# Performance work log

Hardware: AMD Instinct MI355X
Metric: run time of the kernel (lower is better)

## Reference

```python
import jax, jax.numpy as jnp
import numpy as np

B, S, D, H = 2, 2048, 768, 12
Dh = D // H  # attention_head_size = 64
NEG = -1e9


def setup_inputs() -> dict:
    key = jax.random.key(0)
    ks = jax.random.split(key, 10)
    scale = 1.0 / np.sqrt(D).astype(np.float32)
    inp = {
        "hidden_states": jax.random.normal(ks[0], (B, S, D), jnp.float32),
        "Wq": jax.random.normal(ks[1], (D, D), jnp.float32) * scale,
        "bq": jnp.zeros((D,), jnp.float32),
        "Wk": jax.random.normal(ks[2], (D, D), jnp.float32) * scale,
        "bk": jnp.zeros((D,), jnp.float32),
        "Wv": jax.random.normal(ks[3], (D, D), jnp.float32) * scale,
        "bv": jnp.zeros((D,), jnp.float32),
        "Wo": jax.random.normal(ks[4], (D, D), jnp.float32) * scale,
        "bo": jnp.zeros((D,), jnp.float32),
        "mask": jax.random.randint(ks[5], (B, S), 0, 2).astype(bool),
    }
    return inp


def _heads(x):
    # [B,S,D] -> [B,H,S,Dh]
    return x.reshape(B, S, H, Dh).transpose(0, 2, 1, 3)


def reference(hidden_states, Wq, bq, Wk, bk, Wv, bv, Wo, bo, mask):
    q = _heads(hidden_states @ Wq + bq)
    k = _heads(hidden_states @ Wk + bk)
    v = _heads(hidden_states @ Wv + bv)

    # [B,H,S,S] raw scores
    scores = jnp.einsum("bhqd,bhkd->bhqk", q, k) / np.sqrt(Dh).astype(np.float32)

    # pairwise fg mask: [B,1,S,S]; True where both query and key tokens are fg
    am = mask[:, None, :, None] & mask[:, None, None, :]

    # fg softmax: bg pairs masked to -1e9; bg softmax: fg pairs masked to -1e9
    fg_probs = jax.nn.softmax(jnp.where(am, scores, NEG), axis=-1)
    bg_probs = jnp.where(am, NEG, scores)
    bg_probs = jax.nn.softmax(bg_probs, axis=-1)

    # stitch: take fg probs at fg pairs, bg probs elsewhere (replaces boolean scatter)
    probs = jnp.where(am, fg_probs, bg_probs)

    ctx = jnp.einsum("bhqk,bhkd->bhqd", probs, v)
    ctx = ctx.transpose(0, 2, 1, 3).reshape(B, S, D)
    return ctx @ Wo + bo
```

## Files before the change

### kernel.cpp

```cpp
#include <hip/hip_runtime.h>

typedef float f32x4 __attribute__((ext_vector_type(4)));
typedef short bf16x8 __attribute__((ext_vector_type(8)));

#define MFMA16(a, b, c) __builtin_amdgcn_mfma_f32_16x16x32_bf16((a), (b), (c), 0, 0, 0)
#define WAITV4() asm volatile("s_waitcnt vmcnt(4)" ::: "memory")
#define WAITV8() asm volatile("s_waitcnt vmcnt(8)" ::: "memory")
#define WAITV0() asm volatile("s_waitcnt vmcnt(0)" ::: "memory")
#define WAITL0() asm volatile("s_waitcnt lgkmcnt(0)" ::: "memory")
#define BARRIER() __builtin_amdgcn_s_barrier()
#define SCHED0() __builtin_amdgcn_sched_barrier(0)

constexpr int S_ = 2048;
constexpr int D_ = 768;
constexpr int H_ = 12;
constexpr int DH = 64;
constexpr int B_ = 2;
constexpr int M_ = B_ * S_;
constexpr int BH = B_ * H_;

typedef unsigned short u16;
typedef unsigned int u32;

__device__ __forceinline__ u16 f2bf(float f) {
  u32 u = __builtin_bit_cast(u32, f);
  u += 0x7fffu + ((u >> 16) & 1u);
  return (u16)(u >> 16);
}
__device__ __forceinline__ u32 pack2(float a, float b) {
  return (u32)f2bf(a) | ((u32)f2bf(b) << 16);
}
__device__ __forceinline__ u32 pack2r(float lo, float hi) {
  u32 a = __builtin_bit_cast(u32, lo) + 0x8000u;
  u32 b = __builtin_bit_cast(u32, hi) + 0x8000u;
  return __builtin_amdgcn_perm(b, a, 0x07060302u);
}

__device__ __forceinline__ void gload16(const void* g, void* l) {
  __builtin_amdgcn_global_load_lds((const __attribute__((address_space(1))) u32*)g,
                                   (__attribute__((address_space(3))) u32*)l, 16, 0, 0);
}

__global__ __launch_bounds__(256) void conv_bf16(const float* __restrict__ in,
                                                 u16* __restrict__ out) {
  int i = blockIdx.x * 256 + threadIdx.x;
  float4 v = ((const float4*)in)[i];
  uint2 r;
  r.x = pack2(v.x, v.y);
  r.y = pack2(v.z, v.w);
  ((uint2*)out)[i] = r;
}

__global__ __launch_bounds__(256) void conv_wT4(const float* __restrict__ Wq,
                                                const float* __restrict__ Wk,
                                                const float* __restrict__ Wv,
                                                const float* __restrict__ Wo,
                                                u16* __restrict__ wqkv,
                                                u16* __restrict__ wo) {
  __shared__ float t[32][33];
  int z = blockIdx.z;
  const float* w = z == 0 ? Wq : z == 1 ? Wk : z == 2 ? Wv : Wo;
  u16* wt = z == 3 ? wo : wqkv + (size_t)z * D_ * D_;
  int k0 = blockIdx.x << 5, n0 = blockIdx.y << 5;
  int x = threadIdx.x & 31, y = threadIdx.x >> 5;
#pragma unroll
  for (int j = 0; j < 4; ++j) t[y + 8 * j][x] = w[(size_t)(k0 + y + 8 * j) * D_ + n0 + x];
  __syncthreads();
#pragma unroll
  for (int j = 0; j < 4; ++j) wt[(size_t)(n0 + y + 8 * j) * D_ + k0 + x] = f2bf(t[x][y + 8 * j]);
}

__global__ __launch_bounds__(256) void canon_mask(const void* __restrict__ mraw,
                                                  float* __restrict__ fm,
                                                  u32* __restrict__ mw) {
  __shared__ int isBool;
  int tid = threadIdx.x;
  if (tid == 0) isBool = 0;
  __syncthreads();
  const int* mi = (const int*)mraw;
  int v = mi[tid];
  if (v != 0 && v != 1) atomicOr(&isBool, 1);
  __syncthreads();
  const unsigned char* mb = (const unsigned char*)mraw;
  int p = blockIdx.x * 256 + tid;
  int m0, m1;
  if (isBool) { m0 = mb[2 * p]; m1 = mb[2 * p + 1]; }
  else        { m0 = mi[2 * p]; m1 = mi[2 * p + 1]; }
  fm[2 * p] = (float)m0;
  fm[2 * p + 1] = (float)m1;
  mw[p] = (m0 ? 0xFFFFu : 0u) | (m1 ? 0xFFFF0000u : 0u);
}

template <int MODE>
__global__ __launch_bounds__(256, 2) void gemm128(const u16* __restrict__ A,
                                                  const u16* __restrict__ Wt,
                                                  const float* __restrict__ bq,
                                                  const float* __restrict__ bk,
                                                  const float* __restrict__ bv,
                                                  u16* __restrict__ oq,
                                                  u16* __restrict__ ok,
                                                  u16* __restrict__ ov,
                                                  float* __restrict__ of,
                                                  float qscale) {
  constexpr int NT = D_ / 64;
  __shared__ __align__(16) u16 lA[2][128 * 64];
  __shared__ __align__(16) u16 lB[2][128 * 64];
  const int tid = threadIdx.x, w = tid >> 6, lane = tid & 63;
  const int g = lane >> 4, c = lane & 15;
  const int m0 = blockIdx.x * 128, n0 = blockIdx.y * 128;
  const int wr = w >> 1, wc = w & 1;
  const int srow = lane >> 3, scb = ((lane & 7) * 16) ^ (srow << 4);
  const int sw = (c & 7) << 4;
  const char* Ab = (const char*)A + (size_t)m0 * (D_ * 2);
  const char* Bb = (const char*)Wt + (size_t)n0 * (D_ * 2);

  auto stage = [&](int buf, int t) {
    int k0b = t * 128;
#pragma unroll
    for (int a = 0; a < 4; ++a) {
      int rr = w * 32 + a * 8;
      gload16(Ab + (size_t)(rr + srow) * (D_ * 2) + k0b + scb, &lA[buf][rr * 64]);
      gload16(Bb + (size_t)(rr + srow) * (D_ * 2) + k0b + scb, &lB[buf][rr * 64]);
    }
  };

  f32x4 acc[4][4] = {};
  auto compute = [&](int buf) {
    const char* pa = (const char*)&lA[buf][0];
    const char* pb = (const char*)&lB[buf][0];
#pragma unroll
    for (int kk = 0; kk < 2; ++kk) {
      const int cs = (kk * 64 + g * 16) ^ sw;
      bf16x8 af[4], bf[4];
#pragma unroll
      for (int i = 0; i < 4; ++i)
        af[i] = *(const bf16x8*)(pa + (wr * 64 + i * 16 + c) * 128 + cs);
#pragma unroll
      for (int j = 0; j < 4; ++j)
        bf[j] = *(const bf16x8*)(pb + (wc * 64 + j * 16 + c) * 128 + cs);
      __builtin_amdgcn_s_setprio(1);
#pragma unroll
      for (int i = 0; i < 4; ++i)
#pragma unroll
        for (int j = 0; j < 4; ++j) acc[i][j] = MFMA16(af[i], bf[j], acc[i][j]);
      __builtin_amdgcn_s_setprio(0);
    }
  };

  stage(0, 0);
  int buf = 0;
#pragma unroll 1
  for (int t = 0; t < NT; ++t) {
    if (t + 1 < NT) { stage(buf ^ 1, t + 1); WAITV8(); }
    else            { WAITV0(); }
    BARRIER(); SCHED0();
    compute(buf);
    SCHED0(); WAITL0(); BARRIER();
    buf ^= 1;
  }

  if (MODE == 0) {
    const int p = n0 / D_;
    const int nn0 = n0 - p * D_;
    const float* bias = p == 0 ? bq : p == 1 ? bk : bv;
    const float sc = p == 0 ? qscale : 1.0f;
#pragma unroll
    for (int j = 0; j < 4; ++j) {
      int nn = nn0 + wc * 64 + j * 16 + c;
      float bvv = bias[nn];
      int h = nn >> 6, d = nn & 63;
#pragma unroll
      for (int i = 0; i < 4; ++i) {
        int m = m0 + wr * 64 + i * 16 + g * 4;
        int b = m >> 11, s = m & (S_ - 1);
        if (p < 2) {
          u16* dst = (p == 0 ? oq : ok) + ((size_t)(b * H_ + h) * S_ + s) * DH + d;
#pragma unroll
          for (int r = 0; r < 4; ++r) dst[(size_t)r * DH] = f2bf((acc[i][j][r] + bvv) * sc);
        } else {
          int chunk = s >> 5, kq = (s >> 2) & 7;
          int sb = kq < 4 ? 8 * kq : 8 * (kq - 4) + 4;
          uint2 pk;
          pk.x = pack2r(acc[i][j][0] + bvv, acc[i][j][1] + bvv);
          pk.y = pack2r(acc[i][j][2] + bvv, acc[i][j][3] + bvv);
          *(uint2*)(ov + ((size_t)((b * H_ + h) * DH + d)) * S_ + chunk * 32 + sb) = pk;
        }
      }
    }
  } else {
#pragma unroll
    for (int j = 0; j < 4; ++j) {
      int n = n0 + wc * 64 + j * 16 + c;
      float bvv = bq[n];
#pragma unroll
      for (int i = 0; i < 4; ++i) {
        int m = m0 + wr * 64 + i * 16 + g * 4;
#pragma unroll
        for (int r = 0; r < 4; ++r) of[(size_t)(m + r) * D_ + n] = acc[i][j][r] + bvv;
      }
    }
  }
}

__global__ __launch_bounds__(256, 3) void attn(const u16* __restrict__ Q,
                                               const u16* __restrict__ K,
                                               const u16* __restrict__ Vt,
                                               const float* __restrict__ fm,
                                               const u32* __restrict__ mw,
                                               u16* __restrict__ ctx) {
  constexpr int NT = S_ / 64;
  __shared__ __align__(16) char smem[40960];
  char* lKb = smem;
  char* lVb = smem + 16384;
  char* lMb = smem + 32768;

  const int tid = threadIdx.x;
  const int w = tid >> 6, lane = tid & 63;
  const int g = lane >> 4, c = lane & 15;
  const int qh = w & 1, kh = w >> 1;
  const int bid = blockIdx.x;
  const int wg = (bid & 7) * 96 + (bid >> 3);
  const int qt = wg & 31, bh = wg >> 5;
  const int b = bh / H_, h = bh % H_;
  const int qbase = qt * 64 + qh * 32;

  const u16* Qp = Q + ((size_t)bh * S_ + qbase) * DH;
  const char* Kp = (const char*)(K + (size_t)bh * S_ * DH);
  const char* Vp = (const char*)(Vt + (size_t)bh * DH * S_);
  const float* fmp = fm + b * S_;
  const char* mwp = (const char*)(mw + b * (S_ / 2));

  bf16x8 qf[2][2];
#pragma unroll
  for (int qs = 0; qs < 2; ++qs)
#pragma unroll
    for (int kk = 0; kk < 2; ++kk)
      qf[qs][kk] = *(const bf16x8*)(Qp + (qs * 16 + c) * DH + kk * 32 + g * 8);

  u32 ow = (c == 0) ? 0x3F803F80u : 0u;
  uint4 owv = {ow, ow, ow, ow};
  bf16x8 onesf = __builtin_bit_cast(bf16x8, owv);

  const int srow = lane >> 3;
  const int scb = ((lane & 7) * 16) ^ (srow << 4);
  const int sw = (c & 7) << 4;
  const int r8a = w * 2, r8b = w * 2 + 1;
  const int rowA = r8a * 8 + srow, rowB = r8b * 8 + srow;

  f32x4 accf[2][4] = {}, accb[2][4] = {}, alf[2] = {}, alb[2] = {};

  auto stage = [&](int buf, int t) {
    const char* kb_ = Kp + (size_t)t * 8192;
    const char* vb_ = Vp + (size_t)t * 128;
    gload16(kb_ + (size_t)rowA * 128 + scb, lKb + buf * 8192 + r8a * 1024);
    gload16(kb_ + (size_t)rowB * 128 + scb, lKb + buf * 8192 + r8b * 1024);
    gload16(vb_ + (size_t)rowA * 4096 + scb, lVb + buf * 8192 + r8a * 1024);
    gload16(vb_ + (size_t)rowB * 4096 + scb, lVb + buf * 8192 + r8b * 1024);
  };

  auto compute = [&](int buf, int t) {
    const char* kt = lKb + buf * 8192;
    const char* vtl = lVb + buf * 8192;
    const int kc = kh;
    uint2 m01 = *(const uint2*)(lMb + t * 128 + kc * 64 + g * 8);
    uint2 m23 = *(const uint2*)(lMb + t * 128 + kc * 64 + 32 + g * 8);
    bf16x8 k00 = *(const bf16x8*)(kt + (kc * 32 + c) * 128 + ((g * 16) ^ sw));
    bf16x8 k01 = *(const bf16x8*)(kt + (kc * 32 + c) * 128 + ((64 + g * 16) ^ sw));
    bf16x8 k10 = *(const bf16x8*)(kt + (kc * 32 + 16 + c) * 128 + ((g * 16) ^ sw));
    bf16x8 k11 = *(const bf16x8*)(kt + (kc * 32 + 16 + c) * 128 + ((64 + g * 16) ^ sw));
    const int csel = (kc * 64 + g * 16) ^ sw;
    bf16x8 vf0 = *(const bf16x8*)(vtl + (0 * 16 + c) * 128 + csel);
    bf16x8 vf1 = *(const bf16x8*)(vtl + (1 * 16 + c) * 128 + csel);
    bf16x8 vf2 = *(const bf16x8*)(vtl + (2 * 16 + c) * 128 + csel);
    bf16x8 vf3 = *(const bf16x8*)(vtl + (3 * 16 + c) * 128 + csel);
#pragma unroll
    for (int qs = 0; qs < 2; ++qs) {
      f32x4 st0 = {}, st1 = {};
      __builtin_amdgcn_s_setprio(1);
      st0 = MFMA16(k00, qf[qs][0], st0);
      st0 = MFMA16(k01, qf[qs][1], st0);
      st1 = MFMA16(k10, qf[qs][0], st1);
      st1 = MFMA16(k11, qf[qs][1], st1);
      __builtin_amdgcn_s_setprio(0);
      u32 ew0 = pack2r(__builtin_amdgcn_exp2f(st0[0]), __builtin_amdgcn_exp2f(st0[1]));
      u32 ew1 = pack2r(__builtin_amdgcn_exp2f(st0[2]), __builtin_amdgcn_exp2f(st0[3]));
      u32 ew2 = pack2r(__builtin_amdgcn_exp2f(st1[0]), __builtin_amdgcn_exp2f(st1[1]));
      u32 ew3 = pack2r(__builtin_amdgcn_exp2f(st1[2]), __builtin_amdgcn_exp2f(st1[3]));
      u32 pf0 = ew0 & m01.x, pf1 = ew1 & m01.y;
      u32 pf2 = ew2 & m23.x, pf3 = ew3 & m23.y;
      uint4 pfv = {pf0, pf1, pf2, pf3};
      uint4 pbv = {ew0 ^ pf0, ew1 ^ pf1, ew2 ^ pf2, ew3 ^ pf3};
      bf16x8 paf = __builtin_bit_cast(bf16x8, pfv);
      bf16x8 pab = __builtin_bit_cast(bf16x8, pbv);
      __builtin_amdgcn_s_setprio(1);
      accf[qs][0] = MFMA16(paf, vf0, accf[qs][0]);
      accb[qs][0] = MFMA16(pab, vf0, accb[qs][0]);
      accf[qs][1] = MFMA16(paf, vf1, accf[qs][1]);
      accb[qs][1] = MFMA16(pab, vf1, accb[qs][1]);
      accf[qs][2] = MFMA16(paf, vf2, accf[qs][2]);
      accb[qs][2] = MFMA16(pab, vf2, accb[qs][2]);
      accf[qs][3] = MFMA16(paf, vf3, accf[qs][3]);
      accb[qs][3] = MFMA16(pab, vf3, accb[qs][3]);
      alf[qs] = MFMA16(paf, onesf, alf[qs]);
      alb[qs] = MFMA16(pab, onesf, alb[qs]);
      __builtin_amdgcn_s_setprio(0);
    }
  };

  gload16(mwp + w * 1024 + lane * 16, lMb + w * 1024);
  stage(0, 0);

  int buf = 0;
#pragma unroll 1
  for (int t = 0; t < NT; ++t) {
    if (t + 1 < NT) { stage(buf ^ 1, t + 1); WAITV4(); }
    else            { WAITV0(); }
    BARRIER(); SCHED0();
    compute(buf, t);
    SCHED0(); WAITL0(); BARRIER();
    buf ^= 1;
  }

  f32x4* red = (f32x4*)smem + (size_t)qh * 1280;
  if (kh == 1) {
#pragma unroll
    for (int qs = 0; qs < 2; ++qs)
#pragma unroll
      for (int n = 0; n < 4; ++n) {
        red[(qs * 4 + n) * 64 + lane] = accf[qs][n];
        red[(8 + qs * 4 + n) * 64 + lane] = accb[qs][n];
      }
    red[16 * 64 + lane] = alf[0];
    red[17 * 64 + lane] = alf[1];
    red[18 * 64 + lane] = alb[0];
    red[19 * 64 + lane] = alb[1];
  }
  __syncthreads();
  if (kh == 0) {
#pragma unroll
    for (int qs = 0; qs < 2; ++qs)
#pragma unroll
      for (int n = 0; n < 4; ++n) {
        accf[qs][n] += red[(qs * 4 + n) * 64 + lane];
        accb[qs][n] += red[(8 + qs * 4 + n) * 64 + lane];
      }
    alf[0] += red[16 * 64 + lane];
    alf[1] += red[17 * 64 + lane];
    alb[0] += red[18 * 64 + lane];
    alb[1] += red[19 * 64 + lane];

#pragma unroll
    for (int qs = 0; qs < 2; ++qs) {
      const int qw = qbase + qs * 16;
#pragma unroll
      for (int r = 0; r < 4; ++r) {
        int ql = g * 4 + r;
        float lfr = __shfl(alf[qs][r], g * 16);
        float lbr = __shfl(alb[qs][r], g * 16);
        bool fg = fmp[qw + ql] > 0.5f;
        float inv_f = (lfr > 0.f) ? 1.f / lfr : 0.f;
        float inv_b = (lbr > 0.f) ? 1.f / lbr : 0.f;
        float inv_all = 1.f / (lfr + lbr);
#pragma unroll
        for (int n = 0; n < 4; ++n) {
          float o = fg ? (accf[qs][n][r] * inv_f + accb[qs][n][r] * inv_b)
                       : ((accf[qs][n][r] + accb[qs][n][r]) * inv_all);
          ctx[((size_t)(b * S_ + qw + ql)) * D_ + h * DH + n * 16 + c] = f2bf(o);
        }
      }
    }
  }
}

extern "C" void kernel_launch(void* const* d_in, const int* in_sizes, int n_in,
                              void* d_out, int out_size, void* d_ws, size_t ws_size,
                              hipStream_t stream) {
  const float* hs = (const float*)d_in[0];
  const float* Wq = (const float*)d_in[1];
  const float* bq = (const float*)d_in[2];
  const float* Wk = (const float*)d_in[3];
  const float* bk = (const float*)d_in[4];
  const float* Wv = (const float*)d_in[5];
  const float* bv = (const float*)d_in[6];
  const float* Wo = (const float*)d_in[7];
  const float* bo = (const float*)d_in[8];
  const void* mraw = d_in[9];

  char* ws = (char*)d_ws;
  size_t off = 0;
  auto alloc = [&](size_t bytes) {
    void* p = ws + off;
    off += (bytes + 255) & ~(size_t)255;
    return p;
  };
  u16* hsb = (u16*)alloc((size_t)M_ * D_ * 2);
  u16* wqkvT = (u16*)alloc((size_t)3 * D_ * D_ * 2);
  u16* woT = (u16*)alloc((size_t)D_ * D_ * 2);
  u16* qb = (u16*)alloc((size_t)M_ * D_ * 2);
  u16* kb = (u16*)alloc((size_t)M_ * D_ * 2);
  u16* vtb = (u16*)alloc((size_t)M_ * D_ * 2);
  u16* ctx = (u16*)alloc((size_t)M_ * D_ * 2);
  float* fmf = (float*)alloc((size_t)B_ * S_ * 4);
  u32* mwb = (u32*)alloc((size_t)B_ * S_ / 2 * 4);

  conv_bf16<<<(M_ * D_ / 4 + 255) / 256, 256, 0, stream>>>(hs, hsb);
  conv_wT4<<<dim3(D_ / 32, D_ / 32, 4), 256, 0, stream>>>(Wq, Wk, Wv, Wo, wqkvT, woT);
  canon_mask<<<B_ * S_ / 512, 256, 0, stream>>>(mraw, fmf, mwb);

  const float qscale = 0.125f * 1.44269504088896f;
  gemm128<0><<<dim3(M_ / 128, 3 * D_ / 128), 256, 0, stream>>>(
      hsb, wqkvT, bq, bk, bv, qb, kb, vtb, nullptr, qscale);

  attn<<<dim3(768), 256, 0, stream>>>(qb, kb, vtb, fmf, mwb, ctx);

  gemm128<1><<<dim3(M_ / 128, D_ / 128), 256, 0, stream>>>(
      ctx, woT, bo, nullptr, nullptr, nullptr, nullptr, nullptr, (float*)d_out, 1.0f);
}
```

Before: 104.8 us.

## Fuse prep kernels, cut attention LDS for higher occupancy, simplify pipeline sync

```diff
diff --git a/kernel.cpp b/kernel.cpp
--- a/kernel.cpp
+++ b/kernel.cpp
@@ -4,7 +4,6 @@
 typedef short bf16x8 __attribute__((ext_vector_type(8)));
 
 #define MFMA16(a, b, c) __builtin_amdgcn_mfma_f32_16x16x32_bf16((a), (b), (c), 0, 0, 0)
-#define WAITV4() asm volatile("s_waitcnt vmcnt(4)" ::: "memory")
 #define WAITV8() asm volatile("s_waitcnt vmcnt(8)" ::: "memory")
 #define WAITV0() asm volatile("s_waitcnt vmcnt(0)" ::: "memory")
 #define WAITL0() asm volatile("s_waitcnt lgkmcnt(0)" ::: "memory")
@@ -41,54 +40,59 @@
                                    (__attribute__((address_space(3))) u32*)l, 16, 0, 0);
 }
 
-__global__ __launch_bounds__(256) void conv_bf16(const float* __restrict__ in,
-                                                 u16* __restrict__ out) {
-  int i = blockIdx.x * 256 + threadIdx.x;
-  float4 v = ((const float4*)in)[i];
-  uint2 r;
-  r.x = pack2(v.x, v.y);
-  r.y = pack2(v.z, v.w);
-  ((uint2*)out)[i] = r;
-}
-
-__global__ __launch_bounds__(256) void conv_wT4(const float* __restrict__ Wq,
-                                                const float* __restrict__ Wk,
-                                                const float* __restrict__ Wv,
-                                                const float* __restrict__ Wo,
-                                                u16* __restrict__ wqkv,
-                                                u16* __restrict__ wo) {
+constexpr int PREP_NB_CONV = M_ * D_ / 4 / 256;
+constexpr int PREP_NB_W = (D_ / 32) * (D_ / 32) * 4;
+constexpr int PREP_NB_MASK = B_ * S_ / 512;
+__global__ __launch_bounds__(256) void prep(const float* __restrict__ hs,
+                                            const float* __restrict__ Wq,
+                                            const float* __restrict__ Wk,
+                                            const float* __restrict__ Wv,
+                                            const float* __restrict__ Wo,
+                                            u16* __restrict__ hsb,
+                                            u16* __restrict__ wqkv,
+                                            u16* __restrict__ wo,
+                                            const void* __restrict__ mraw,
+                                            float* __restrict__ fm,
+                                            u32* __restrict__ mw) {
   __shared__ float t[32][33];
-  int z = blockIdx.z;
-  const float* w = z == 0 ? Wq : z == 1 ? Wk : z == 2 ? Wv : Wo;
-  u16* wt = z == 3 ? wo : wqkv + (size_t)z * D_ * D_;
-  int k0 = blockIdx.x << 5, n0 = blockIdx.y << 5;
-  int x = threadIdx.x & 31, y = threadIdx.x >> 5;
-#pragma unroll
-  for (int j = 0; j < 4; ++j) t[y + 8 * j][x] = w[(size_t)(k0 + y + 8 * j) * D_ + n0 + x];
-  __syncthreads();
-#pragma unroll
-  for (int j = 0; j < 4; ++j) wt[(size_t)(n0 + y + 8 * j) * D_ + k0 + x] = f2bf(t[x][y + 8 * j]);
-}
-
-__global__ __launch_bounds__(256) void canon_mask(const void* __restrict__ mraw,
-                                                  float* __restrict__ fm,
-                                                  u32* __restrict__ mw) {
   __shared__ int isBool;
-  int tid = threadIdx.x;
-  if (tid == 0) isBool = 0;
-  __syncthreads();
-  const int* mi = (const int*)mraw;
-  int v = mi[tid];
-  if (v != 0 && v != 1) atomicOr(&isBool, 1);
-  __syncthreads();
-  const unsigned char* mb = (const unsigned char*)mraw;
-  int p = blockIdx.x * 256 + tid;
-  int m0, m1;
-  if (isBool) { m0 = mb[2 * p]; m1 = mb[2 * p + 1]; }
-  else        { m0 = mi[2 * p]; m1 = mi[2 * p + 1]; }
-  fm[2 * p] = (float)m0;
-  fm[2 * p + 1] = (float)m1;
-  mw[p] = (m0 ? 0xFFFFu : 0u) | (m1 ? 0xFFFF0000u : 0u);
+  const int bid = blockIdx.x, tid = threadIdx.x;
+  if (bid < PREP_NB_CONV) {
+    int i = bid * 256 + tid;
+    float4 v = ((const float4*)hs)[i];
+    uint2 r;
+    r.x = pack2(v.x, v.y);
+    r.y = pack2(v.z, v.w);
+    ((uint2*)hsb)[i] = r;
+  } else if (bid < PREP_NB_CONV + PREP_NB_W) {
+    int zz = bid - PREP_NB_CONV;
+    int z = zz / 576, r = zz % 576;
+    int kx = r % 24, ny = r / 24;
+    const float* w = z == 0 ? Wq : z == 1 ? Wk : z == 2 ? Wv : Wo;
+    u16* wt = z == 3 ? wo : wqkv + (size_t)z * D_ * D_;
+    int k0 = kx << 5, n0 = ny << 5;
+    int x = tid & 31, y = tid >> 5;
+#pragma unroll
+    for (int j = 0; j < 4; ++j) t[y + 8 * j][x] = w[(size_t)(k0 + y + 8 * j) * D_ + n0 + x];
+    __syncthreads();
+#pragma unroll
+    for (int j = 0; j < 4; ++j) wt[(size_t)(n0 + y + 8 * j) * D_ + k0 + x] = f2bf(t[x][y + 8 * j]);
+  } else {
+    if (tid == 0) isBool = 0;
+    __syncthreads();
+    const int* mi = (const int*)mraw;
+    int v = mi[tid];
+    if (v != 0 && v != 1) atomicOr(&isBool, 1);
+    __syncthreads();
+    const unsigned char* mb = (const unsigned char*)mraw;
+    int p = (bid - PREP_NB_CONV - PREP_NB_W) * 256 + tid;
+    int m0, m1;
+    if (isBool) { m0 = mb[2 * p]; m1 = mb[2 * p + 1]; }
+    else        { m0 = mi[2 * p]; m1 = mi[2 * p + 1]; }
+    fm[2 * p] = (float)m0;
+    fm[2 * p + 1] = (float)m1;
+    mw[p] = (m0 ? 0xFFFFu : 0u) | (m1 ? 0xFFFF0000u : 0u);
+  }
 }
 
 template <int MODE>
@@ -202,17 +206,16 @@
   }
 }
 
-__global__ __launch_bounds__(256, 3) void attn(const u16* __restrict__ Q,
+__global__ __launch_bounds__(256, 4) void attn(const u16* __restrict__ Q,
                                                const u16* __restrict__ K,
                                                const u16* __restrict__ Vt,
                                                const float* __restrict__ fm,
                                                const u32* __restrict__ mw,
                                                u16* __restrict__ ctx) {
   constexpr int NT = S_ / 64;
-  __shared__ __align__(16) char smem[40960];
+  __shared__ __align__(16) char smem[32768];
   char* lKb = smem;
   char* lVb = smem + 16384;
-  char* lMb = smem + 32768;
 
   const int tid = threadIdx.x;
   const int w = tid >> 6, lane = tid & 63;
@@ -228,7 +231,7 @@
   const char* Kp = (const char*)(K + (size_t)bh * S_ * DH);
   const char* Vp = (const char*)(Vt + (size_t)bh * DH * S_);
   const float* fmp = fm + b * S_;
-  const char* mwp = (const char*)(mw + b * (S_ / 2));
+  const char* mwp = (const char*)(mw + b * (S_ / 2)) + kh * 64 + g * 8;
 
   bf16x8 qf[2][2];
 #pragma unroll
@@ -262,8 +265,8 @@
     const char* kt = lKb + buf * 8192;
     const char* vtl = lVb + buf * 8192;
     const int kc = kh;
-    uint2 m01 = *(const uint2*)(lMb + t * 128 + kc * 64 + g * 8);
-    uint2 m23 = *(const uint2*)(lMb + t * 128 + kc * 64 + 32 + g * 8);
+    uint2 m01 = *(const uint2*)(mwp + (size_t)t * 128);
+    uint2 m23 = *(const uint2*)(mwp + (size_t)t * 128 + 32);
     bf16x8 k00 = *(const bf16x8*)(kt + (kc * 32 + c) * 128 + ((g * 16) ^ sw));
     bf16x8 k01 = *(const bf16x8*)(kt + (kc * 32 + c) * 128 + ((64 + g * 16) ^ sw));
     bf16x8 k10 = *(const bf16x8*)(kt + (kc * 32 + 16 + c) * 128 + ((g * 16) ^ sw));
@@ -307,48 +310,52 @@
     }
   };
 
-  gload16(mwp + w * 1024 + lane * 16, lMb + w * 1024);
   stage(0, 0);
+  __syncthreads();
 
   int buf = 0;
 #pragma unroll 1
   for (int t = 0; t < NT; ++t) {
-    if (t + 1 < NT) { stage(buf ^ 1, t + 1); WAITV4(); }
-    else            { WAITV0(); }
-    BARRIER(); SCHED0();
+    if (t + 1 < NT) stage(buf ^ 1, t + 1);
     compute(buf, t);
-    SCHED0(); WAITL0(); BARRIER();
+    __syncthreads();
     buf ^= 1;
   }
 
-  f32x4* red = (f32x4*)smem + (size_t)qh * 1280;
-  if (kh == 1) {
-#pragma unroll
-    for (int qs = 0; qs < 2; ++qs)
-#pragma unroll
-      for (int n = 0; n < 4; ++n) {
-        red[(qs * 4 + n) * 64 + lane] = accf[qs][n];
-        red[(8 + qs * 4 + n) * 64 + lane] = accb[qs][n];
-      }
-    red[16 * 64 + lane] = alf[0];
-    red[17 * 64 + lane] = alf[1];
-    red[18 * 64 + lane] = alb[0];
-    red[19 * 64 + lane] = alb[1];
-  }
-  __syncthreads();
+  f32x4* red = (f32x4*)smem;
+#pragma unroll 1
+  for (int ph = 0; ph < 2; ++ph) {
+    if (qh == ph && kh == 1) {
+#pragma unroll
+      for (int qs = 0; qs < 2; ++qs)
+#pragma unroll
+        for (int n = 0; n < 4; ++n) {
+          red[(qs * 4 + n) * 64 + lane] = accf[qs][n];
+          red[(8 + qs * 4 + n) * 64 + lane] = accb[qs][n];
+        }
+      red[16 * 64 + lane] = alf[0];
+      red[17 * 64 + lane] = alf[1];
+      red[18 * 64 + lane] = alb[0];
+      red[19 * 64 + lane] = alb[1];
+    }
+    __syncthreads();
+    if (qh == ph && kh == 0) {
+#pragma unroll
+      for (int qs = 0; qs < 2; ++qs)
+#pragma unroll
+        for (int n = 0; n < 4; ++n) {
+          accf[qs][n] += red[(qs * 4 + n) * 64 + lane];
+          accb[qs][n] += red[(8 + qs * 4 + n) * 64 + lane];
+        }
+      alf[0] += red[16 * 64 + lane];
+      alf[1] += red[17 * 64 + lane];
+      alb[0] += red[18 * 64 + lane];
+      alb[1] += red[19 * 64 + lane];
+    }
+    __syncthreads();
+  }
+
   if (kh == 0) {
-#pragma unroll
-    for (int qs = 0; qs < 2; ++qs)
-#pragma unroll
-      for (int n = 0; n < 4; ++n) {
-        accf[qs][n] += red[(qs * 4 + n) * 64 + lane];
-        accb[qs][n] += red[(8 + qs * 4 + n) * 64 + lane];
-      }
-    alf[0] += red[16 * 64 + lane];
-    alf[1] += red[17 * 64 + lane];
-    alb[0] += red[18 * 64 + lane];
-    alb[1] += red[19 * 64 + lane];
-
 #pragma unroll
     for (int qs = 0; qs < 2; ++qs) {
       const int qw = qbase + qs * 16;
@@ -403,9 +410,8 @@
   float* fmf = (float*)alloc((size_t)B_ * S_ * 4);
   u32* mwb = (u32*)alloc((size_t)B_ * S_ / 2 * 4);
 
-  conv_bf16<<<(M_ * D_ / 4 + 255) / 256, 256, 0, stream>>>(hs, hsb);
-  conv_wT4<<<dim3(D_ / 32, D_ / 32, 4), 256, 0, stream>>>(Wq, Wk, Wv, Wo, wqkvT, woT);
-  canon_mask<<<B_ * S_ / 512, 256, 0, stream>>>(mraw, fmf, mwb);
+  prep<<<PREP_NB_CONV + PREP_NB_W + PREP_NB_MASK, 256, 0, stream>>>(
+      hs, Wq, Wk, Wv, Wo, hsb, wqkvT, woT, mraw, fmf, mwb);
 
   const float qscale = 0.125f * 1.44269504088896f;
   gemm128<0><<<dim3(M_ / 128, 3 * D_ / 128), 256, 0, stream>>>(
```

Measured after the change: 246.1 us. 2.35x slower.
